# Kernel optimization log

Hardware: AMD Instinct MI355X
Metric: run time of the kernel (lower is better)

## Reference

```python
import jax, jax.numpy as jnp
import numpy as np

EPS = 1e-6
H = 12  # num_attention_heads

def _phi(x):
    # feature map used by fast-transformers LinearAttention: elu(x) + 1
    return jax.nn.elu(x) + 1.0

def setup_inputs() -> dict:
    key = jax.random.key(0)
    k1, k2, k3 = jax.random.split(key, 3)
    B, N, D = 32, 1024, 768
    x = jax.random.normal(k1, (B, N, D), dtype=jnp.float32)
    W_qkv = jax.random.normal(k2, (D, 3 * D), dtype=jnp.float32) * (D ** -0.5)
    W_out = jax.random.normal(k3, (D, D), dtype=jnp.float32) * (D ** -0.5)
    b_out = jnp.zeros((D,), dtype=jnp.float32)
    return {"x": x, "W_qkv": W_qkv, "W_out": W_out, "b_out": b_out}

def reference(x, W_qkv, W_out, b_out):
    B, N, D = x.shape
    d = D // H
    # F.pad(x, [0,0,0,1]): append one zero token along sequence
    x_ = jnp.pad(x, ((0, 0), (0, 1), (0, 0)))              # [B, N+1, D]
    qkv = x_ @ W_qkv                                        # [B, N+1, 3D]
    q, k, v = jnp.split(qkv, 3, axis=-1)
    q = q.reshape(B, N + 1, H, d)
    k = k.reshape(B, N + 1, H, d)
    v = v.reshape(B, N + 1, H, d)
    # non-causal linear attention (mask is all-ones -> no masking)
    q = _phi(q)
    k = _phi(k)
    kv = jnp.einsum('bshd,bshm->bhdm', k, v)                # [B, H, d, d]
    z = 1.0 / (jnp.einsum('blhd,bhd->blh', q, k.sum(axis=1)) + EPS)
    out = jnp.einsum('blhd,bhdm,blh->blhm', q, kv, z)       # [B, N+1, H, d]
    out = out.reshape(B, N + 1, D)
    out = out @ W_out + b_out                               # dropout = identity (eval)
    return out[:, :-1, :]                                   # drop padding token
```

## Files before the change

### kernel.cpp

```cpp
#include <hip/hip_runtime.h>
#include <hip/hip_bf16.h>


typedef __bf16 bf16x8 __attribute__((ext_vector_type(8)));
typedef float f32x4 __attribute__((ext_vector_type(4)));

__device__ __forceinline__ ushort f2bf(float f) {
  union { float f; unsigned u; } x; x.f = f;
  unsigned r = x.u + 0x7fffu + ((x.u >> 16) & 1u);
  return (ushort)(r >> 16);
}
__device__ __forceinline__ float bf2f(ushort h) {
  union { unsigned u; float f; } x; x.u = ((unsigned)h) << 16;
  return x.f;
}
__device__ __forceinline__ void gload_lds16(const void* g, void* lds) {
  __builtin_amdgcn_global_load_lds((const __attribute__((address_space(1))) void*)g,
                                   (__attribute__((address_space(3))) void*)lds, 16, 0, 0);
}

__global__ __launch_bounds__(256) void cvt_f32_bf16(const float* __restrict__ in,
                                                    ushort* __restrict__ out, int n4) {
  int i = blockIdx.x * 256 + threadIdx.x;
  if (i >= n4) return;
  float4 v = reinterpret_cast<const float4*>(in)[i];
  ushort4 o;
  o.x = f2bf(v.x); o.y = f2bf(v.y); o.z = f2bf(v.z); o.w = f2bf(v.w);
  reinterpret_cast<ushort4*>(out)[i] = o;
}

__global__ __launch_bounds__(256) void transpose_cvt(const float* __restrict__ src,
                                                     ushort* __restrict__ dst, int R, int C) {
  __shared__ float tile[32][33];
  int bc = blockIdx.x * 32, br = blockIdx.y * 32;
  int tx = threadIdx.x & 31, ty = threadIdx.x >> 5;
  #pragma unroll
  for (int i = 0; i < 32; i += 8)
    tile[ty + i][tx] = src[(size_t)(br + ty + i) * C + (bc + tx)];
  __syncthreads();
  #pragma unroll
  for (int i = 0; i < 32; i += 8)
    dst[(size_t)(bc + ty + i) * R + (br + tx)] = f2bf(tile[tx][ty + i]);
}

template <int MODE>
__global__ __launch_bounds__(512, 2) void gemm256(const ushort* __restrict__ A,
                                                  const ushort* __restrict__ Bt,
                                                  void* __restrict__ C,
                                                  const float* __restrict__ bias,
                                                  int N, int K, int nbx, int cpx) {
  extern __shared__ ushort lds[];
  const int tid = threadIdx.x;
  const int lane = tid & 63;
  const int wid = tid >> 6;
  const int wm = wid >> 2, wn = wid & 3;
  const int laneR = lane & 15, laneS = lane >> 4;

  const int bid = blockIdx.x;
  const int lin = (bid & 7) * cpx + (bid >> 3);
  const int by = lin / nbx, bx = lin - by * nbx;
  const int m0 = by * 256, n0 = bx * 256;
  const int NT = K >> 6;

  const int sr = tid >> 2, ss = tid & 3;
  const int sslot = ss ^ ((sr >> 1) & 3);
  const ushort* Asrc0 = A + (size_t)(m0 + sr) * K + sslot * 8;
  const ushort* Bsrc0 = Bt + (size_t)(n0 + sr) * K + sslot * 8;
  const size_t rowstep = (size_t)128 * K;
  const int ldst0 = tid * 8;

  const int sprime = laneS ^ ((laneR >> 1) & 3);
  const int aoff = (wm * 128 + laneR) * 32 + sprime * 8;
  const int boff = 16384 + (wn * 64 + laneR) * 32 + sprime * 8;

  f32x4 acc[8][4] = {};

  #define STAGE_HT(SRC, KT, KS, DST)                                              \
    { gload_lds16((SRC) + (KT) * 64 + (KS) * 32,                                  \
                  (DST) + (KS) * 8192 + ldst0);                                   \
      gload_lds16((SRC) + (KT) * 64 + (KS) * 32 + rowstep,                        \
                  (DST) + (KS) * 8192 + 4096 + ldst0); }

  {
    ushort* b0 = lds;
    ushort* b1 = lds + 32768;
    STAGE_HT(Asrc0, 0, 0, b0);
    STAGE_HT(Bsrc0, 0, 0, b0 + 16384);
    STAGE_HT(Asrc0, 0, 1, b0);
    STAGE_HT(Bsrc0, 0, 1, b0 + 16384);
    STAGE_HT(Asrc0, 1, 0, b1);
    STAGE_HT(Bsrc0, 1, 0, b1 + 16384);
  }
  asm volatile("s_waitcnt vmcnt(8)" ::: "memory");
  __builtin_amdgcn_sched_barrier(0);
  __builtin_amdgcn_s_barrier();
  __builtin_amdgcn_sched_barrier(0);

  for (int t = 0; t < NT; ++t) {
    ushort* cbuf = lds + (t & 1) * 32768;
    ushort* nbuf = lds + ((t & 1) ^ 1) * 32768;
    const int t1 = (t + 1 < NT) ? t + 1 : t;
    const int t2 = (t + 2 < NT) ? t + 2 : t;
    bf16x8 afr[4], bfr[4];

    #pragma unroll
    for (int j = 0; j < 4; ++j)
      bfr[j] = *(const bf16x8*)(cbuf + boff + j * 512);
    #pragma unroll
    for (int ii = 0; ii < 4; ++ii)
      afr[ii] = *(const bf16x8*)(cbuf + aoff + ii * 512);
    STAGE_HT(Asrc0, t1, 1, nbuf);
    __builtin_amdgcn_sched_barrier(0);
    __builtin_amdgcn_s_barrier();
    __builtin_amdgcn_s_setprio(1);
    #pragma unroll
    for (int ii = 0; ii < 4; ++ii)
      #pragma unroll
      for (int j = 0; j < 4; ++j)
        acc[ii][j] = __builtin_amdgcn_mfma_f32_16x16x32_bf16(afr[ii], bfr[j], acc[ii][j], 0, 0, 0);
    __builtin_amdgcn_s_setprio(0);
    __builtin_amdgcn_s_barrier();
    __builtin_amdgcn_sched_barrier(0);

    #pragma unroll
    for (int ii = 0; ii < 4; ++ii)
      afr[ii] = *(const bf16x8*)(cbuf + aoff + (4 + ii) * 512);
    STAGE_HT(Bsrc0, t1, 1, nbuf + 16384);
    asm volatile("s_waitcnt vmcnt(8)" ::: "memory");
    __builtin_amdgcn_sched_barrier(0);
    __builtin_amdgcn_s_barrier();
    __builtin_amdgcn_s_setprio(1);
    #pragma unroll
    for (int ii = 0; ii < 4; ++ii)
      #pragma unroll
      for (int j = 0; j < 4; ++j)
        acc[4 + ii][j] = __builtin_amdgcn_mfma_f32_16x16x32_bf16(afr[ii], bfr[j], acc[4 + ii][j], 0, 0, 0);
    __builtin_amdgcn_s_setprio(0);
    __builtin_amdgcn_s_barrier();
    __builtin_amdgcn_sched_barrier(0);

    #pragma unroll
    for (int j = 0; j < 4; ++j)
      bfr[j] = *(const bf16x8*)(cbuf + 8192 + boff + j * 512);
    #pragma unroll
    for (int ii = 0; ii < 4; ++ii)
      afr[ii] = *(const bf16x8*)(cbuf + 8192 + aoff + ii * 512);
    STAGE_HT(Asrc0, t2, 0, cbuf);
    __builtin_amdgcn_sched_barrier(0);
    __builtin_amdgcn_s_barrier();
    __builtin_amdgcn_s_setprio(1);
    #pragma unroll
    for (int ii = 0; ii < 4; ++ii)
      #pragma unroll
      for (int j = 0; j < 4; ++j)
        acc[ii][j] = __builtin_amdgcn_mfma_f32_16x16x32_bf16(afr[ii], bfr[j], acc[ii][j], 0, 0, 0);
    __builtin_amdgcn_s_setprio(0);
    __builtin_amdgcn_s_barrier();
    __builtin_amdgcn_sched_barrier(0);

    #pragma unroll
    for (int ii = 0; ii < 4; ++ii)
      afr[ii] = *(const bf16x8*)(cbuf + 8192 + aoff + (4 + ii) * 512);
    STAGE_HT(Bsrc0, t2, 0, cbuf + 16384);
    asm volatile("s_waitcnt vmcnt(8)" ::: "memory");
    __builtin_amdgcn_sched_barrier(0);
    __builtin_amdgcn_s_barrier();
    __builtin_amdgcn_s_setprio(1);
    #pragma unroll
    for (int ii = 0; ii < 4; ++ii)
      #pragma unroll
      for (int j = 0; j < 4; ++j)
        acc[4 + ii][j] = __builtin_amdgcn_mfma_f32_16x16x32_bf16(afr[ii], bfr[j], acc[4 + ii][j], 0, 0, 0);
    __builtin_amdgcn_s_setprio(0);
    __builtin_amdgcn_s_barrier();
    __builtin_amdgcn_sched_barrier(0);
  }
  #undef STAGE_HT
  asm volatile("s_waitcnt vmcnt(0)" ::: "memory");

  #pragma unroll
  for (int i = 0; i < 8; ++i) {
    const int grow0 = m0 + wm * 128 + i * 16 + (laneS << 2);
    #pragma unroll
    for (int j = 0; j < 4; ++j) {
      const int gcol = n0 + wn * 64 + j * 16 + laneR;
      #pragma unroll
      for (int r = 0; r < 4; ++r) {
        float v = acc[i][j][r];
        if (MODE == 0) {
          if (gcol < 1536) v = (v > 0.f) ? (v + 1.f) : __expf(v);
          reinterpret_cast<ushort*>(C)[(size_t)(grow0 + r) * N + gcol] = f2bf(v);
        } else {
          reinterpret_cast<float*>(C)[(size_t)(grow0 + r) * N + gcol] = v + bias[gcol];
        }
      }
    }
  }
}

__global__ __launch_bounds__(256) void kv_partial(const ushort* __restrict__ qkv,
                                                  float* __restrict__ kv_part,
                                                  float* __restrict__ ks_part) {
  const int blk = blockIdx.x;
  const int bh = blk >> 2, sp = blk & 3;
  const int b = bh / 12, h = bh % 12;
  const int tid = threadIdx.x;
  __shared__ ushort Ks[32 * 64];
  __shared__ ushort Vs[32 * 64];
  float acc[4][4] = {};
  float kacc[4] = {};
  const int dq0 = (tid & 15) * 4, mq0 = (tid >> 4) * 4;
  const int r = tid >> 3, o = tid & 7;
  for (int st = 0; st < 256; st += 32) {
    const int s0 = sp * 256 + st;
    __syncthreads();
    const size_t rowbase = (size_t)(b * 1024 + s0 + r) * 2304 + h * 64 + o * 8;
    gload_lds16(qkv + rowbase + 768,  &Ks[tid * 8]);
    gload_lds16(qkv + rowbase + 1536, &Vs[tid * 8]);
    asm volatile("s_waitcnt vmcnt(0)" ::: "memory");
    __syncthreads();
    #pragma unroll 8
    for (int s = 0; s < 32; ++s) {
      short4 kk = *reinterpret_cast<const short4*>(&Ks[s * 64 + dq0]);
      short4 vv = *reinterpret_cast<const short4*>(&Vs[s * 64 + mq0]);
      float kf[4] = { bf2f((ushort)kk.x), bf2f((ushort)kk.y), bf2f((ushort)kk.z), bf2f((ushort)kk.w) };
      float vf[4] = { bf2f((ushort)vv.x), bf2f((ushort)vv.y), bf2f((ushort)vv.z), bf2f((ushort)vv.w) };
      #pragma unroll
      for (int jm = 0; jm < 4; ++jm)
        #pragma unroll
        for (int id = 0; id < 4; ++id)
          acc[jm][id] += vf[jm] * kf[id];
      if (mq0 == 0) {
        #pragma unroll
        for (int id = 0; id < 4; ++id) kacc[id] += kf[id];
      }
    }
  }
  float* kvp = kv_part + ((size_t)sp * 384 + bh) * 4096;
  #pragma unroll
  for (int jm = 0; jm < 4; ++jm)
    #pragma unroll
    for (int id = 0; id < 4; ++id)
      kvp[(mq0 + jm) * 64 + dq0 + id] = acc[jm][id];
  if (mq0 == 0) {
    #pragma unroll
    for (int id = 0; id < 4; ++id)
      ks_part[((size_t)sp * 384 + bh) * 64 + dq0 + id] = kacc[id];
  }
}

__global__ __launch_bounds__(256) void kv_reduce(const float* __restrict__ kv_part,
                                                 const float* __restrict__ ks_part,
                                                 ushort* __restrict__ kv_bf,
                                                 float* __restrict__ ksum) {
  int i = blockIdx.x * 256 + threadIdx.x;
  if (i < 384 * 4096) {
    float s = 0.f;
    #pragma unroll
    for (int p = 0; p < 4; ++p) s += kv_part[(size_t)p * (384 * 4096) + i];
    kv_bf[i] = f2bf(s);
  }
  if (i < 384 * 64) {
    float s = 1.0f;
    #pragma unroll
    for (int p = 0; p < 4; ++p) s += ks_part[(size_t)p * (384 * 64) + i];
    ksum[i] = s;
  }
}

__global__ __launch_bounds__(256) void attn_kernel(const ushort* __restrict__ qkv,
                                                   const ushort* __restrict__ kv_bf,
                                                   const float* __restrict__ ksum,
                                                   ushort* __restrict__ attn) {
  const int blk = blockIdx.x;
  const int bh = blk >> 3, tb = blk & 7;
  const int b = bh / 12, h = bh % 12;
  const int row0 = b * 1024 + tb * 128;
  __shared__ ushort Qs[128 * 64];
  __shared__ ushort KVs[64 * 64];
  __shared__ float zs[128];
  __shared__ float ks_lds[64];
  const int tid = threadIdx.x;
  const int lane = tid & 63, w = tid >> 6;
  #pragma unroll
  for (int j = 0; j < 4; ++j) {
    int c = j * 256 + tid;
    gload_lds16(qkv + (size_t)(row0 + (c >> 3)) * 2304 + h * 64 + (c & 7) * 8, &Qs[c * 8]);
  }
  #pragma unroll
  for (int j = 0; j < 2; ++j) {
    int c = j * 256 + tid;
    gload_lds16(kv_bf + (size_t)bh * 4096 + c * 8, &KVs[c * 8]);
  }
  if (tid < 64) ks_lds[tid] = ksum[bh * 64 + tid];
  asm volatile("s_waitcnt vmcnt(0)" ::: "memory");
  __syncthreads();
  if (tid < 128) {
    float d = 0.f;
    #pragma unroll 8
    for (int e = 0; e < 64; ++e) d += bf2f(Qs[tid * 64 + e]) * ks_lds[e];
    zs[tid] = 1.f / (d + 1e-6f);
  }
  __syncthreads();
  f32x4 acc[2][4] = {};
  #pragma unroll
  for (int ks = 0; ks < 2; ++ks) {
    bf16x8 a[2], bb[4];
    #pragma unroll
    for (int i = 0; i < 2; ++i)
      a[i] = *reinterpret_cast<const bf16x8*>(&Qs[(w * 32 + i * 16 + (lane & 15)) * 64 + ks * 32 + (lane >> 4) * 8]);
    #pragma unroll
    for (int j = 0; j < 4; ++j)
      bb[j] = *reinterpret_cast<const bf16x8*>(&KVs[(j * 16 + (lane & 15)) * 64 + ks * 32 + (lane >> 4) * 8]);
    #pragma unroll
    for (int i = 0; i < 2; ++i)
      #pragma unroll
      for (int j = 0; j < 4; ++j)
        acc[i][j] = __builtin_amdgcn_mfma_f32_16x16x32_bf16(a[i], bb[j], acc[i][j], 0, 0, 0);
  }
  #pragma unroll
  for (int i = 0; i < 2; ++i) {
    const int t0 = w * 32 + i * 16 + ((lane >> 4) << 2);
    #pragma unroll
    for (int j = 0; j < 4; ++j) {
      const int m = j * 16 + (lane & 15);
      #pragma unroll
      for (int r = 0; r < 4; ++r) {
        float v = acc[i][j][r] * zs[t0 + r];
        attn[(size_t)(row0 + t0 + r) * 768 + h * 64 + m] = f2bf(v);
      }
    }
  }
}

extern "C" void kernel_launch(void* const* d_in, const int* in_sizes, int n_in,
                              void* d_out, int out_size, void* d_ws, size_t ws_size,
                              hipStream_t stream) {
  (void)in_sizes; (void)n_in; (void)out_size; (void)ws_size;
  const float* x    = (const float*)d_in[0];
  const float* Wqkv = (const float*)d_in[1];
  const float* Wout = (const float*)d_in[2];
  const float* bout = (const float*)d_in[3];
  float* out = (float*)d_out;
  char* ws = (char*)d_ws;

  ushort* xbf    = (ushort*)(ws);
  ushort* wqkvT  = (ushort*)(ws + 50331648);
  ushort* woutT  = (ushort*)(ws + 53870592);
  ushort* qkv    = (ushort*)(ws + 55050240);
  float*  ksp    = (float*) (ws + 206045184);
  ushort* kvbf   = (ushort*)(ws + 206438400);
  float*  ksum   = (float*) (ws + 209584128);
  float*  kvpart = (float*)(ws);
  ushort* attn   = (ushort*)(ws);

  static const int LDS_BYTES = 131072;
  hipFuncSetAttribute(reinterpret_cast<const void*>(&gemm256<0>),
                      hipFuncAttributeMaxDynamicSharedMemorySize, LDS_BYTES);
  hipFuncSetAttribute(reinterpret_cast<const void*>(&gemm256<1>),
                      hipFuncAttributeMaxDynamicSharedMemorySize, LDS_BYTES);

  cvt_f32_bf16<<<24576, 256, 0, stream>>>(x, xbf, 6291456);
  transpose_cvt<<<dim3(72, 24), 256, 0, stream>>>(Wqkv, wqkvT, 768, 2304);
  transpose_cvt<<<dim3(24, 24), 256, 0, stream>>>(Wout, woutT, 768, 768);
  gemm256<0><<<1152, 512, LDS_BYTES, stream>>>(xbf, wqkvT, qkv, nullptr, 2304, 768, 9, 144);
  kv_partial<<<1536, 256, 0, stream>>>(qkv, kvpart, ksp);
  kv_reduce<<<6144, 256, 0, stream>>>(kvpart, ksp, kvbf, ksum);
  attn_kernel<<<3072, 256, 0, stream>>>(qkv, kvbf, ksum, attn);
  gemm256<1><<<384, 512, LDS_BYTES, stream>>>(attn, woutT, out, bout, 768, 768, 3, 48);
}
```

Before: 316.8 us.

## Double-buffer MFMA operand registers to overlap LDS reads with matrix math

Restructures the GEMM main loop so A/B fragments for the next sub-step are read from LDS into a second register set while MFMAs run on the current set, with fragments preloaded before the loop. The goal is to hide LDS read latency behind MFMA execution instead of serializing fragment loads before each compute phase. The vmcnt waits change placement and count, and the extra fragment registers raise register pressure. Correctness depends on the reordered waits and barriers still covering the async global-to-LDS copies.

```diff
diff --git a/kernel.cpp b/kernel.cpp
--- a/kernel.cpp
+++ b/kernel.cpp
@@ -74,12 +74,21 @@
   const int boff = 16384 + (wn * 64 + laneR) * 32 + sprime * 8;
 
   f32x4 acc[8][4] = {};
+  bf16x8 afrX[4], afrY[4], bfrX[4], bfrY[4];
 
   #define STAGE_HT(SRC, KT, KS, DST)                                              \
     { gload_lds16((SRC) + (KT) * 64 + (KS) * 32,                                  \
                   (DST) + (KS) * 8192 + ldst0);                                   \
       gload_lds16((SRC) + (KT) * 64 + (KS) * 32 + rowstep,                        \
                   (DST) + (KS) * 8192 + 4096 + ldst0); }
+  #define SBAR  __builtin_amdgcn_sched_barrier(0)
+  #define MFMA16(ACCBASE, AF, BF)                                                 \
+    _Pragma("unroll")                                                             \
+    for (int ii = 0; ii < 4; ++ii)                                                \
+      _Pragma("unroll")                                                           \
+      for (int j = 0; j < 4; ++j)                                                 \
+        acc[(ACCBASE) + ii][j] =                                                  \
+            __builtin_amdgcn_mfma_f32_16x16x32_bf16(AF[ii], BF[j], acc[(ACCBASE) + ii][j], 0, 0, 0);
 
   {
     ushort* b0 = lds;
@@ -92,90 +101,84 @@
     STAGE_HT(Bsrc0, 1, 0, b1 + 16384);
   }
   asm volatile("s_waitcnt vmcnt(8)" ::: "memory");
-  __builtin_amdgcn_sched_barrier(0);
+  SBAR;
   __builtin_amdgcn_s_barrier();
-  __builtin_amdgcn_sched_barrier(0);
+  SBAR;
+  #pragma unroll
+  for (int j = 0; j < 4; ++j)
+    bfrX[j] = *(const bf16x8*)(lds + boff + j * 512);
+  #pragma unroll
+  for (int ii = 0; ii < 4; ++ii)
+    afrX[ii] = *(const bf16x8*)(lds + aoff + ii * 512);
 
   for (int t = 0; t < NT; ++t) {
     ushort* cbuf = lds + (t & 1) * 32768;
     ushort* nbuf = lds + ((t & 1) ^ 1) * 32768;
     const int t1 = (t + 1 < NT) ? t + 1 : t;
     const int t2 = (t + 2 < NT) ? t + 2 : t;
-    bf16x8 afr[4], bfr[4];
-
+
+    STAGE_HT(Asrc0, t1, 1, nbuf);
+    asm volatile("s_waitcnt vmcnt(6)" ::: "memory");
+    SBAR;
+    #pragma unroll
+    for (int ii = 0; ii < 4; ++ii)
+      afrY[ii] = *(const bf16x8*)(cbuf + aoff + (4 + ii) * 512);
+    SBAR;
+    __builtin_amdgcn_s_setprio(1);
+    MFMA16(0, afrX, bfrX);
+    __builtin_amdgcn_s_setprio(0);
+    SBAR;
+    __builtin_amdgcn_s_barrier();
+    SBAR;
+
+    STAGE_HT(Bsrc0, t1, 1, nbuf + 16384);
+    SBAR;
     #pragma unroll
     for (int j = 0; j < 4; ++j)
-      bfr[j] = *(const bf16x8*)(cbuf + boff + j * 512);
+      bfrY[j] = *(const bf16x8*)(cbuf + 8192 + boff + j * 512);
     #pragma unroll
     for (int ii = 0; ii < 4; ++ii)
-      afr[ii] = *(const bf16x8*)(cbuf + aoff + ii * 512);
-    STAGE_HT(Asrc0, t1, 1, nbuf);
-    __builtin_amdgcn_sched_barrier(0);
+      afrX[ii] = *(const bf16x8*)(cbuf + 8192 + aoff + ii * 512);
+    SBAR;
+    __builtin_amdgcn_s_setprio(1);
+    MFMA16(4, afrY, bfrX);
+    __builtin_amdgcn_s_setprio(0);
+    SBAR;
     __builtin_amdgcn_s_barrier();
+    SBAR;
+
+    STAGE_HT(Asrc0, t2, 0, cbuf);
+    asm volatile("s_waitcnt vmcnt(6)" ::: "memory");
+    SBAR;
+    #pragma unroll
+    for (int ii = 0; ii < 4; ++ii)
+      afrY[ii] = *(const bf16x8*)(cbuf + 8192 + aoff + (4 + ii) * 512);
+    SBAR;
     __builtin_amdgcn_s_setprio(1);
+    MFMA16(0, afrX, bfrY);
+    __builtin_amdgcn_s_setprio(0);
+    SBAR;
+    __builtin_amdgcn_s_barrier();
+    SBAR;
+
+    STAGE_HT(Bsrc0, t2, 0, cbuf + 16384);
+    SBAR;
+    #pragma unroll
+    for (int j = 0; j < 4; ++j)
+      bfrX[j] = *(const bf16x8*)(nbuf + boff + j * 512);
     #pragma unroll
     for (int ii = 0; ii < 4; ++ii)
-      #pragma unroll
-      for (int j = 0; j < 4; ++j)
-        acc[ii][j] = __builtin_amdgcn_mfma_f32_16x16x32_bf16(afr[ii], bfr[j], acc[ii][j], 0, 0, 0);
+      afrX[ii] = *(const bf16x8*)(nbuf + aoff + ii * 512);
+    SBAR;
+    __builtin_amdgcn_s_setprio(1);
+    MFMA16(4, afrY, bfrY);
     __builtin_amdgcn_s_setprio(0);
+    SBAR;
     __builtin_amdgcn_s_barrier();
-    __builtin_amdgcn_sched_barrier(0);
-
-    #pragma unroll
-    for (int ii = 0; ii < 4; ++ii)
-      afr[ii] = *(const bf16x8*)(cbuf + aoff + (4 + ii) * 512);
-    STAGE_HT(Bsrc0, t1, 1, nbuf + 16384);
-    asm volatile("s_waitcnt vmcnt(8)" ::: "memory");
-    __builtin_amdgcn_sched_barrier(0);
-    __builtin_amdgcn_s_barrier();
-    __builtin_amdgcn_s_setprio(1);
-    #pragma unroll
-    for (int ii = 0; ii < 4; ++ii)
-      #pragma unroll
-      for (int j = 0; j < 4; ++j)
-        acc[4 + ii][j] = __builtin_amdgcn_mfma_f32_16x16x32_bf16(afr[ii], bfr[j], acc[4 + ii][j], 0, 0, 0);
-    __builtin_amdgcn_s_setprio(0);
-    __builtin_amdgcn_s_barrier();
-    __builtin_amdgcn_sched_barrier(0);
-
-    #pragma unroll
-    for (int j = 0; j < 4; ++j)
-      bfr[j] = *(const bf16x8*)(cbuf + 8192 + boff + j * 512);
-    #pragma unroll
-    for (int ii = 0; ii < 4; ++ii)
-      afr[ii] = *(const bf16x8*)(cbuf + 8192 + aoff + ii * 512);
-    STAGE_HT(Asrc0, t2, 0, cbuf);
-    __builtin_amdgcn_sched_barrier(0);
-    __builtin_amdgcn_s_barrier();
-    __builtin_amdgcn_s_setprio(1);
-    #pragma unroll
-    for (int ii = 0; ii < 4; ++ii)
-      #pragma unroll
-      for (int j = 0; j < 4; ++j)
-        acc[ii][j] = __builtin_amdgcn_mfma_f32_16x16x32_bf16(afr[ii], bfr[j], acc[ii][j], 0, 0, 0);
-    __builtin_amdgcn_s_setprio(0);
-    __builtin_amdgcn_s_barrier();
-    __builtin_amdgcn_sched_barrier(0);
-
-    #pragma unroll
-    for (int ii = 0; ii < 4; ++ii)
-      afr[ii] = *(const bf16x8*)(cbuf + 8192 + aoff + (4 + ii) * 512);
-    STAGE_HT(Bsrc0, t2, 0, cbuf + 16384);
-    asm volatile("s_waitcnt vmcnt(8)" ::: "memory");
-    __builtin_amdgcn_sched_barrier(0);
-    __builtin_amdgcn_s_barrier();
-    __builtin_amdgcn_s_setprio(1);
-    #pragma unroll
-    for (int ii = 0; ii < 4; ++ii)
-      #pragma unroll
-      for (int j = 0; j < 4; ++j)
-        acc[4 + ii][j] = __builtin_amdgcn_mfma_f32_16x16x32_bf16(afr[ii], bfr[j], acc[4 + ii][j], 0, 0, 0);
-    __builtin_amdgcn_s_setprio(0);
-    __builtin_amdgcn_s_barrier();
-    __builtin_amdgcn_sched_barrier(0);
+    SBAR;
   }
   #undef STAGE_HT
+  #undef MFMA16
   asm volatile("s_waitcnt vmcnt(0)" ::: "memory");
 
   #pragma unroll
```

Result: no change. 315.6 us (-0.4%).
